# Kernel tuning notes

Measured on AMD Instinct MI355X. Metric: run time of the kernel, lower is better.

The kernel has to match this reference:

```python
import jax, jax.numpy as jnp
import numpy as np

D = 128        # embed_d
L = 2          # n_layers
B = 4096       # batch of center nodes (drugs)
S = 10         # num_samples per neighbor type (hard-coded in node_het_agg)
NUM_CELLS, NUM_DRUGS, NUM_GENES = 2000, 4000, 20000
DRUG_F, GENE_F = 1024, 2048
NT = 3         # node types: cell, drug, gene


def setup_inputs() -> dict:
    key = jax.random.key(0)
    ks = jax.random.split(key, 16)
    s = 0.02
    inp = {
        # raw per-type feature tables (feature_loader / embedding table)
        "drug_feats": jax.random.normal(ks[0], (NUM_DRUGS, DRUG_F), jnp.float32),
        "gene_feats": jax.random.normal(ks[1], (NUM_GENES, GENE_F), jnp.float32),
        "cell_tab": jax.random.normal(ks[2], (NUM_CELLS, D), jnp.float32) * s,
        # feat_proj linears
        "W_drug": jax.random.normal(ks[3], (DRUG_F, D), jnp.float32) * s,
        "b_drug": jnp.zeros((D,), jnp.float32),
        "W_gene": jax.random.normal(ks[4], (GENE_F, D), jnp.float32) * s,
        "b_gene": jnp.zeros((D,), jnp.float32),
        # RnnGnnLayer params: per layer, per neighbor type, a simple tanh RNN
        "rnn_Wx": jax.random.normal(ks[5], (L, NT, D, D), jnp.float32) * s,
        "rnn_Wh": jax.random.normal(ks[6], (L, NT, D, D), jnp.float32) * s,
        "rnn_b": jnp.zeros((L, NT, D), jnp.float32),
        # per-layer attention vector over [self || candidate]
        "att_w": jax.random.normal(ks[7], (L, 2 * D), jnp.float32) * s,
        # center node ids (drug type) and pre-sampled neighbor ids per layer/type
        "center_ids": jax.random.randint(ks[8], (B,), 0, NUM_DRUGS, jnp.int32),
        "cell_neigh": jax.random.randint(ks[9], (L, B, S), 0, NUM_CELLS, jnp.int32),
        "drug_neigh": jax.random.randint(ks[10], (L, B, S), 0, NUM_DRUGS, jnp.int32),
        "gene_neigh": jax.random.randint(ks[11], (L, B, S), 0, NUM_GENES, jnp.int32),
    }
    return inp


def reference(drug_feats, gene_feats, cell_tab, W_drug, b_drug, W_gene, b_gene,
              rnn_Wx, rnn_Wh, rnn_b, att_w,
              center_ids, cell_neigh, drug_neigh, gene_neigh):
    # conteng_agg per node type: gather raw features then project to embed_d
    def emb_cell(idx):
        return cell_tab[idx]                              # [..., D]

    def emb_drug(idx):
        return drug_feats[idx] @ W_drug + b_drug          # gather [..., DRUG_F] -> [..., D]

    def emb_gene(idx):
        return gene_feats[idx] @ W_gene + b_gene

    def rnn_agg(x, Wx, Wh, b):
        # x: [B, S, D]; simple tanh RNN over the S sampled neighbors, last hidden
        def step(h, xt):
            h = jnp.tanh(xt @ Wx + h @ Wh + b)
            return h, None
        h0 = jnp.zeros((x.shape[0], Wx.shape[1]), x.dtype)
        h_last, _ = jax.lax.scan(step, h0, jnp.swapaxes(x, 0, 1))
        return h_last                                      # [B, D]

    h = emb_drug(center_ids)                               # initial center embeds [B, D]
    n_layers = rnn_Wx.shape[0]
    for l in range(n_layers):
        neigh = [(cell_neigh[l], emb_cell), (drug_neigh[l], emb_drug), (gene_neigh[l], emb_gene)]
        aggs = []
        for t, (idx, emb) in enumerate(neigh):
            x = emb(idx)                                   # [B, S, D]
            aggs.append(rnn_agg(x, rnn_Wx[l, t], rnn_Wh[l, t], rnn_b[l, t]))
        cands = jnp.stack([h] + aggs, axis=1)              # [B, 1+NT, D]
        self_b = jnp.broadcast_to(h[:, None, :], cands.shape)
        scores = jax.nn.leaky_relu(jnp.concatenate([self_b, cands], axis=-1) @ att_w[l])  # [B, 1+NT]
        alpha = jax.nn.softmax(scores, axis=1)
        h = jnp.einsum('bc,bcd->bd', alpha, cands)         # attention-weighted combine
    return h                                               # [B, D]
```

## Files before the change

kernel.cpp:

```cpp
#include <hip/hip_runtime.h>
#include <stdint.h>

#define D 128
#define Ssz 10
#define HP 136
#define NB 4096

typedef uint16_t u16;
typedef uint32_t u32;
typedef __attribute__((ext_vector_type(8))) short short8;
typedef __attribute__((ext_vector_type(4))) float f32x4;

#define AS1U32(p) ((const __attribute__((address_space(1))) u32*)(p))
#define AS3U32(p) ((__attribute__((address_space(3))) u32*)(p))

__device__ __forceinline__ u16 f2bf(float f){
  u32 x = __float_as_uint(f);
  return (u16)((x + 0x7fffu + ((x >> 16) & 1u)) >> 16);
}
__device__ __forceinline__ float bf2f(u16 u){ return __uint_as_float(((u32)u) << 16); }

__device__ __forceinline__ float ftanh(float x){
  float e = __expf(2.0f * x);
  return 1.0f - 2.0f / (e + 1.0f);
}

__global__ __launch_bounds__(256) void prep_kernel(
    const float* __restrict__ W_drug, const float* __restrict__ W_gene,
    const float* __restrict__ rnn_Wx, const float* __restrict__ rnn_Wh,
    const float* __restrict__ cell_tab,
    u16* __restrict__ WdT, u16* __restrict__ WgT,
    u16* __restrict__ WxT6, u16* __restrict__ WhT6,
    u16* __restrict__ cellT)
{
  int i = blockIdx.x * 256 + threadIdx.x;
  if (i < 131072){
    int n = i >> 10, k = i & 1023;
    WdT[i] = f2bf(W_drug[k * D + n]);
  } else if (i < 393216){
    int j = i - 131072;
    int n = j >> 11, k = j & 2047;
    WgT[j] = f2bf(W_gene[k * D + n]);
  } else if (i < 491520){
    int j = i - 393216;
    int n = (j >> 7) & 127, k = j & 127;
    WxT6[j] = f2bf(rnn_Wx[(j & ~16383) + k * D + n]);
  } else if (i < 589824){
    int j = i - 491520;
    int n = (j >> 7) & 127, k = j & 127;
    WhT6[j] = f2bf(rnn_Wh[(j & ~16383) + k * D + n]);
  } else {
    int j = i - 589824;
    float v0 = cell_tab[2 * j], v1 = cell_tab[2 * j + 1];
    ((u32*)cellT)[j] = (u32)f2bf(v0) | ((u32)f2bf(v1) << 16);
  }
}

__global__ __launch_bounds__(256, 2) void proj_gemm(
    const float* __restrict__ feats, int K, int M,
    const u16* __restrict__ WT,
    const float* __restrict__ bias,
    const u16* __restrict__ Wx0,
    const u16* __restrict__ Wx1,
    const float* __restrict__ rb0,
    const float* __restrict__ rb1,
    float* __restrict__ xw0,
    float* __restrict__ xw1,
    float* __restrict__ outf)
{
  __shared__ u16 Bt[128 * 128];

  int lane = threadIdx.x & 63;
  int wave = threadIdx.x >> 6;
  int quad = lane >> 4, l16 = lane & 15;
  int wrow = (wave & 1) * 16;
  int wcol = (wave >> 1) * 64;
  int m0 = blockIdx.x * 32;

  int row = min(m0 + wrow + l16, M - 1);
  const float* aptr = feats + (long)row * K + quad * 8;

  int st_nrow = wave * 32 + (lane >> 4);
  int st_p    = lane & 15;

  f32x4 acc[4];
#pragma unroll
  for (int nt = 0; nt < 4; ++nt){
    float bv = bias[wcol + nt * 16 + l16];
    f32x4 t = {bv, bv, bv, bv};
    acc[nt] = t;
  }

  f32x4 afA[4][2], afB[4][2];
#pragma unroll
  for (int ks = 0; ks < 4; ++ks){
    afA[ks][0] = *(const f32x4*)(aptr + ks * 32);
    afA[ks][1] = *(const f32x4*)(aptr + ks * 32 + 4);
  }

  auto chunk_step = [&](f32x4 (&acur)[4][2], f32x4 (&anxt)[4][2], int kc) {
#pragma unroll
    for (int j = 0; j < 8; ++j){
      int n = st_nrow + j * 4;
      int c = st_p ^ (n & 15);
      const u16* g = WT + (long)n * K + kc + c * 8;
      __builtin_amdgcn_global_load_lds(AS1U32(g),
                                       AS3U32(&Bt[(wave * 8 + j) * 512]),
                                       16, 0, 0);
    }
    if (kc + 128 < K){
#pragma unroll
      for (int ks = 0; ks < 4; ++ks){
        anxt[ks][0] = *(const f32x4*)(aptr + kc + 128 + ks * 32);
        anxt[ks][1] = *(const f32x4*)(aptr + kc + 128 + ks * 32 + 4);
      }
    }
    __syncthreads();

#pragma unroll
    for (int ks = 0; ks < 4; ++ks){
      short8 a;
#pragma unroll
      for (int q = 0; q < 4; ++q){
        a[q]     = (short)f2bf(acur[ks][0][q]);
        a[4 + q] = (short)f2bf(acur[ks][1][q]);
      }
#pragma unroll
      for (int nt = 0; nt < 4; ++nt){
        int n = wcol + nt * 16 + l16;
        int p = (ks * 4 + quad) ^ l16;
        short8 b = *(const short8*)(&Bt[n * 128 + p * 8]);
        acc[nt] = __builtin_amdgcn_mfma_f32_16x16x32_bf16(a, b, acc[nt], 0, 0, 0);
      }
    }
    __syncthreads();
  };

  for (int kc = 0; kc < K; kc += 256){
    chunk_step(afA, afB, kc);
    chunk_step(afB, afA, kc + 128);
  }

  if (outf){
#pragma unroll
    for (int nt = 0; nt < 4; ++nt){
      int col = wcol + nt * 16 + l16;
#pragma unroll
      for (int r = 0; r < 4; ++r){
        int mr = m0 + wrow + quad * 4 + r;
        if (mr < M) outf[(long)mr * D + col] = acc[nt][r];
      }
    }
  }

  u16* Pl = Bt + (wave & 1) * 2176;
#pragma unroll
  for (int nt = 0; nt < 4; ++nt)
#pragma unroll
    for (int r = 0; r < 4; ++r)
      Pl[(quad * 4 + r) * HP + wcol + nt * 16 + l16] = f2bf(acc[nt][r]);
  __syncthreads();

  short8 paf[4];
#pragma unroll
  for (int ks = 0; ks < 4; ++ks)
    paf[ks] = *(const short8*)(&Pl[l16 * HP + ks * 32 + quad * 8]);

  auto xw_pass = [&](const u16* Wx, const float* rb, float* xw){
    f32x4 ac2[4];
#pragma unroll
    for (int nt = 0; nt < 4; ++nt){
      float bv = rb[wcol + nt * 16 + l16];
      f32x4 tv = {bv, bv, bv, bv};
      ac2[nt] = tv;
    }
#pragma unroll
    for (int nt = 0; nt < 4; ++nt){
#pragma unroll
      for (int ks = 0; ks < 4; ++ks){
        short8 b = *(const short8*)(Wx + (wcol + nt * 16 + l16) * D + ks * 32 + quad * 8);
        ac2[nt] = __builtin_amdgcn_mfma_f32_16x16x32_bf16(paf[ks], b, ac2[nt], 0, 0, 0);
      }
    }
#pragma unroll
    for (int nt = 0; nt < 4; ++nt){
      int col = wcol + nt * 16 + l16;
#pragma unroll
      for (int r = 0; r < 4; ++r){
        int mr = m0 + (wave & 1) * 16 + quad * 4 + r;
        if (mr < M) xw[(long)mr * D + col] = ac2[nt][r];
      }
    }
  };
  xw_pass(Wx0, rb0, xw0);
  xw_pass(Wx1, rb1, xw1);
}

__global__ __launch_bounds__(256) void xw_cell(
    const u16* __restrict__ cellT,
    const u16* __restrict__ WxT6,
    const float* __restrict__ bvec,
    float* __restrict__ xwb)
{
  int l = blockIdx.y;
  int mat = l * 3;
  const u16* WT = WxT6 + (size_t)mat * 16384;

  int lane = threadIdx.x & 63, wave = threadIdx.x >> 6;
  int quad = lane >> 4, l16 = lane & 15;
  int mt = blockIdx.x * 64 + wave * 16;
  int mr = min(mt + l16, 1999);

  short8 a[4];
#pragma unroll
  for (int ks = 0; ks < 4; ++ks)
    a[ks] = *(const short8*)(cellT + (long)mr * D + ks * 32 + quad * 8);

  f32x4 acc[8];
#pragma unroll
  for (int nt = 0; nt < 8; ++nt){
    float bv = bvec[mat * D + nt * 16 + l16];
    f32x4 tv = {bv, bv, bv, bv};
    acc[nt] = tv;
  }
#pragma unroll
  for (int nt = 0; nt < 8; ++nt){
#pragma unroll
    for (int ks = 0; ks < 4; ++ks){
      short8 b = *(const short8*)(WT + (nt * 16 + l16) * D + ks * 32 + quad * 8);
      acc[nt] = __builtin_amdgcn_mfma_f32_16x16x32_bf16(a[ks], b, acc[nt], 0, 0, 0);
    }
  }
#pragma unroll
  for (int nt = 0; nt < 8; ++nt){
    int col = nt * 16 + l16;
#pragma unroll
    for (int r = 0; r < 4; ++r){
      int mrow = mt + quad * 4 + r;
      if (mrow < 2000)
        xwb[((long)l * 26000 + mrow) * D + col] = acc[nt][r];
    }
  }
}

__global__ __launch_bounds__(256, 3) void rnn6_kernel(
    const float* __restrict__ xwb,
    const u16* __restrict__ WhT6,
    const int* __restrict__ cn, const int* __restrict__ dn,
    const int* __restrict__ gn,
    u16* __restrict__ agg)
{
  __shared__ u16 hbuf[16 * HP];

  int t = blockIdx.y, l = blockIdx.z;
  const int* idx = (t == 0) ? cn : (t == 1) ? dn : gn;
  int rbase = (t == 0) ? 0 : (t == 1) ? 2000 : 6000;
  int nmax  = (t == 0) ? 2000 : (t == 1) ? 4000 : 20000;
  const float* xw = xwb + ((size_t)l * 26000 + rbase) * D;
  const u16* WT = WhT6 + (size_t)(l * 3 + t) * 16384;

  int tid = threadIdx.x, lane = tid & 63, wave = tid >> 6;
  int quad = lane >> 4, l16 = lane & 15;
  int n0 = wave * 32;

  short8 whf[2][4];
#pragma unroll
  for (int nt = 0; nt < 2; ++nt){
    int n = n0 + nt * 16 + l16;
#pragma unroll
    for (int ks = 0; ks < 4; ++ks)
      whf[nt][ks] = *(const short8*)(WT + n * D + ks * 32 + quad * 8);
  }

  for (int i = tid; i < 16 * HP; i += 256) hbuf[i] = 0;

  int brow = blockIdx.x * 16;
  const int* ip = idx + ((size_t)l * NB + brow + quad * 4) * Ssz;
  long arow = ((long)(l * 3 + t) * NB + brow) * D;

  int nidA[4], nidB[4];
  float xwA[8], xwB[8];
#pragma unroll
  for (int r = 0; r < 4; ++r) nidA[r] = min(max(ip[r * Ssz], 0), nmax - 1);
#pragma unroll
  for (int r = 0; r < 4; ++r){
    const float* p = xw + (long)nidA[r] * D + n0 + l16;
    xwA[r] = p[0]; xwA[4 + r] = p[16];
  }
#pragma unroll
  for (int r = 0; r < 4; ++r) nidB[r] = min(max(ip[r * Ssz + 1], 0), nmax - 1);
  __syncthreads();

  auto step = [&](int s, float (&xwc)[8], int (&nidn)[4],
                  float (&xwn)[8], int (&nidf)[4]){
    if (s + 1 < Ssz){
#pragma unroll
      for (int r = 0; r < 4; ++r){
        const float* p = xw + (long)nidn[r] * D + n0 + l16;
        xwn[r] = p[0]; xwn[4 + r] = p[16];
      }
    }
    if (s + 2 < Ssz){
#pragma unroll
      for (int r = 0; r < 4; ++r)
        nidf[r] = min(max(ip[r * Ssz + s + 2], 0), nmax - 1);
    }
    short8 hf[4];
#pragma unroll
    for (int ks = 0; ks < 4; ++ks)
      hf[ks] = *(const short8*)(&hbuf[l16 * HP + ks * 32 + quad * 8]);
    f32x4 acc0 = {xwc[0], xwc[1], xwc[2], xwc[3]};
    f32x4 acc1 = {xwc[4], xwc[5], xwc[6], xwc[7]};
#pragma unroll
    for (int ks = 0; ks < 4; ++ks){
      acc0 = __builtin_amdgcn_mfma_f32_16x16x32_bf16(hf[ks], whf[0][ks], acc0, 0, 0, 0);
      acc1 = __builtin_amdgcn_mfma_f32_16x16x32_bf16(hf[ks], whf[1][ks], acc1, 0, 0, 0);
    }
    __syncthreads();
#pragma unroll
    for (int r = 0; r < 4; ++r){
      float v0 = ftanh(acc0[r]);
      float v1 = ftanh(acc1[r]);
      hbuf[(quad * 4 + r) * HP + n0 + l16]      = f2bf(v0);
      hbuf[(quad * 4 + r) * HP + n0 + 16 + l16] = f2bf(v1);
      if (s == Ssz - 1){
        long o = arow + (long)(quad * 4 + r) * D;
        agg[o + n0 + l16]      = f2bf(v0);
        agg[o + n0 + 16 + l16] = f2bf(v1);
      }
    }
    __syncthreads();
  };

  step(0, xwA, nidB, xwB, nidA);
  step(1, xwB, nidA, xwA, nidB);
  step(2, xwA, nidB, xwB, nidA);
  step(3, xwB, nidA, xwA, nidB);
  step(4, xwA, nidB, xwB, nidA);
  step(5, xwB, nidA, xwA, nidB);
  step(6, xwA, nidB, xwB, nidA);
  step(7, xwB, nidA, xwA, nidB);
  step(8, xwA, nidB, xwB, nidA);
  step(9, xwB, nidA, xwA, nidB);
}

__global__ __launch_bounds__(256) void att2_kernel(
    const float* __restrict__ drugPf,
    const int* __restrict__ center_ids,
    const u16* __restrict__ agg,
    const float* __restrict__ att_w,
    float* __restrict__ out)
{
  int gt = blockIdx.x * 256 + threadIdx.x;
  int lane = gt & 63;
  int b = gt >> 6;
  int e = 2 * lane;

  int row = min(max(center_ids[b], 0), 3999);
  float h0 = drugPf[(long)row * D + e];
  float h1 = drugPf[(long)row * D + e + 1];

#pragma unroll
  for (int l = 0; l < 2; ++l){
    float c[4][2];
    c[0][0] = h0; c[0][1] = h1;
#pragma unroll
    for (int t = 0; t < 3; ++t){
      long o = ((long)(l * 3 + t) * NB + b) * D + e;
      c[t + 1][0] = bf2f(agg[o]);
      c[t + 1][1] = bf2f(agg[o + 1]);
    }
    const float* aw = att_w + l * 2 * D;
    float as0 = aw[e],     as1 = aw[e + 1];
    float ac0 = aw[D + e], ac1 = aw[D + e + 1];

    float selfp = c[0][0] * as0 + c[0][1] * as1;
    float sc[4];
#pragma unroll
    for (int cc = 0; cc < 4; ++cc) sc[cc] = selfp + c[cc][0] * ac0 + c[cc][1] * ac1;
#pragma unroll
    for (int off = 32; off >= 1; off >>= 1){
#pragma unroll
      for (int cc = 0; cc < 4; ++cc) sc[cc] += __shfl_xor(sc[cc], off, 64);
    }
#pragma unroll
    for (int cc = 0; cc < 4; ++cc) sc[cc] = sc[cc] > 0.f ? sc[cc] : 0.01f * sc[cc];

    float mx = fmaxf(fmaxf(sc[0], sc[1]), fmaxf(sc[2], sc[3]));
    float ex[4], ssum = 0.f;
#pragma unroll
    for (int cc = 0; cc < 4; ++cc){ ex[cc] = expf(sc[cc] - mx); ssum += ex[cc]; }
    float o0 = 0.f, o1 = 0.f;
#pragma unroll
    for (int cc = 0; cc < 4; ++cc){
      float a = ex[cc] / ssum;
      o0 += a * c[cc][0];
      o1 += a * c[cc][1];
    }
    h0 = o0; h1 = o1;
  }
  out[(long)b * D + e]     = h0;
  out[(long)b * D + e + 1] = h1;
}

extern "C" void kernel_launch(void* const* d_in, const int* in_sizes, int n_in,
                              void* d_out, int out_size, void* d_ws, size_t ws_size,
                              hipStream_t stream)
{
  const float* drug_feats = (const float*)d_in[0];
  const float* gene_feats = (const float*)d_in[1];
  const float* cell_tab   = (const float*)d_in[2];
  const float* W_drug     = (const float*)d_in[3];
  const float* b_drug     = (const float*)d_in[4];
  const float* W_gene     = (const float*)d_in[5];
  const float* b_gene     = (const float*)d_in[6];
  const float* rnn_Wx     = (const float*)d_in[7];
  const float* rnn_Wh     = (const float*)d_in[8];
  const float* rnn_b      = (const float*)d_in[9];
  const float* att_w      = (const float*)d_in[10];
  const int* center_ids   = (const int*)d_in[11];
  const int* cell_neigh   = (const int*)d_in[12];
  const int* drug_neigh   = (const int*)d_in[13];
  const int* gene_neigh   = (const int*)d_in[14];

  u16* ws     = (u16*)d_ws;
  u16* WdT    = ws;
  u16* WgT    = WdT + 131072;
  u16* WxT6   = WgT + 262144;
  u16* WhT6   = WxT6 + 98304;
  u16* cellT  = WhT6 + 98304;
  float* drugPf = (float*)(cellT + 256000);
  float* xwb    = drugPf + 512000;
  u16* agg      = (u16*)(xwb + 6656000);

  float* h = (float*)d_out;

  prep_kernel<<<2804, 256, 0, stream>>>(W_drug, W_gene, rnn_Wx, rnn_Wh, cell_tab,
                                        WdT, WgT, WxT6, WhT6, cellT);

  proj_gemm<<<125, 256, 0, stream>>>(drug_feats, 1024, 4000, WdT, b_drug,
                                     WxT6 + 1 * 16384, WxT6 + 4 * 16384,
                                     rnn_b + 1 * D,    rnn_b + 4 * D,
                                     xwb + (size_t)(0 * 26000 + 2000) * D,
                                     xwb + (size_t)(1 * 26000 + 2000) * D,
                                     drugPf);
  proj_gemm<<<625, 256, 0, stream>>>(gene_feats, 2048, 20000, WgT, b_gene,
                                     WxT6 + 2 * 16384, WxT6 + 5 * 16384,
                                     rnn_b + 2 * D,    rnn_b + 5 * D,
                                     xwb + (size_t)(0 * 26000 + 6000) * D,
                                     xwb + (size_t)(1 * 26000 + 6000) * D,
                                     (float*)nullptr);

  xw_cell<<<dim3(32, 2), 256, 0, stream>>>(cellT, WxT6, rnn_b, xwb);

  rnn6_kernel<<<dim3(NB / 16, 3, 2), 256, 0, stream>>>(
      xwb, WhT6, cell_neigh, drug_neigh, gene_neigh, agg);

  att2_kernel<<<NB / 4, 256, 0, stream>>>(drugPf, center_ids, agg, att_w, h);
}
```

Baseline: 365.7 us.

## Double-buffer weight tiles in LDS to overlap staging with MFMA compute

The projection GEMM now keeps two 32KB shared-memory buffers for the weight tile. The next tile is staged by async global-to-LDS copies while the MFMAs run on the current buffer, which removes one barrier per chunk and hides load latency. The cost is doubling LDS to 64KB per block, which may cut occupancy from the requested two blocks per CU.

```diff
diff --git a/kernel.cpp b/kernel.cpp
--- a/kernel.cpp
+++ b/kernel.cpp
@@ -68,7 +68,7 @@
     float* __restrict__ xw1,
     float* __restrict__ outf)
 {
-  __shared__ u16 Bt[128 * 128];
+  __shared__ u16 Bt[2][128 * 128];
 
   int lane = threadIdx.x & 63;
   int wave = threadIdx.x >> 6;
@@ -92,31 +92,26 @@
   }
 
   f32x4 afA[4][2], afB[4][2];
-#pragma unroll
-  for (int ks = 0; ks < 4; ++ks){
-    afA[ks][0] = *(const f32x4*)(aptr + ks * 32);
-    afA[ks][1] = *(const f32x4*)(aptr + ks * 32 + 4);
-  }
-
-  auto chunk_step = [&](f32x4 (&acur)[4][2], f32x4 (&anxt)[4][2], int kc) {
+
+  auto stageB = [&](int buf, int kc){
 #pragma unroll
     for (int j = 0; j < 8; ++j){
       int n = st_nrow + j * 4;
       int c = st_p ^ (n & 15);
       const u16* g = WT + (long)n * K + kc + c * 8;
       __builtin_amdgcn_global_load_lds(AS1U32(g),
-                                       AS3U32(&Bt[(wave * 8 + j) * 512]),
+                                       AS3U32(&Bt[buf][(wave * 8 + j) * 512]),
                                        16, 0, 0);
     }
-    if (kc + 128 < K){
-#pragma unroll
-      for (int ks = 0; ks < 4; ++ks){
-        anxt[ks][0] = *(const f32x4*)(aptr + kc + 128 + ks * 32);
-        anxt[ks][1] = *(const f32x4*)(aptr + kc + 128 + ks * 32 + 4);
-      }
-    }
-    __syncthreads();
-
+  };
+  auto loadA = [&](f32x4 (&af)[4][2], int kc){
+#pragma unroll
+    for (int ks = 0; ks < 4; ++ks){
+      af[ks][0] = *(const f32x4*)(aptr + kc + ks * 32);
+      af[ks][1] = *(const f32x4*)(aptr + kc + ks * 32 + 4);
+    }
+  };
+  auto compute = [&](int buf, f32x4 (&acur)[4][2]){
 #pragma unroll
     for (int ks = 0; ks < 4; ++ks){
       short8 a;
@@ -129,16 +124,27 @@
       for (int nt = 0; nt < 4; ++nt){
         int n = wcol + nt * 16 + l16;
         int p = (ks * 4 + quad) ^ l16;
-        short8 b = *(const short8*)(&Bt[n * 128 + p * 8]);
+        short8 b = *(const short8*)(&Bt[buf][n * 128 + p * 8]);
         acc[nt] = __builtin_amdgcn_mfma_f32_16x16x32_bf16(a, b, acc[nt], 0, 0, 0);
       }
     }
+  };
+
+  stageB(0, 0);
+  loadA(afA, 0);
+  __syncthreads();
+
+  for (int kc = 0; kc < K; kc += 256){
+    stageB(1, kc + 128);
+    loadA(afB, kc + 128);
+    compute(0, afA);
     __syncthreads();
-  };
-
-  for (int kc = 0; kc < K; kc += 256){
-    chunk_step(afA, afB, kc);
-    chunk_step(afB, afA, kc + 128);
+    if (kc + 256 < K){
+      stageB(0, kc + 256);
+      loadA(afA, kc + 256);
+    }
+    compute(1, afB);
+    __syncthreads();
   }
 
   if (outf){
@@ -153,7 +159,7 @@
     }
   }
 
-  u16* Pl = Bt + (wave & 1) * 2176;
+  u16* Pl = &Bt[0][0] + (wave & 1) * 2176;
 #pragma unroll
   for (int nt = 0; nt < 4; ++nt)
 #pragma unroll
```

After: 367.4 us. No clear change (+0.5%).
